# Kernel tuning notes

Measured on AMD Instinct MI355X. Metric: run time of the kernel, lower is better.

## Reference

```python
import jax, jax.numpy as jnp
import numpy as np

H = 4      # attention heads in HGTConv
DH = 32    # head dim
D = 128    # hidden size (rnn.hidden_size == hidden_size)
PAD = 0    # pad_idx


def setup_inputs() -> dict:
    key = jax.random.key(0)
    ks = jax.random.split(key, 16)
    Na = Np = 50000
    E = 800000
    V = 10000
    L = 8
    s = 0.05  # init scale keeps attention logits stable
    return {
        "tok_author": jax.random.randint(ks[0], (Na, L), 0, V),
        "tok_paper": jax.random.randint(ks[1], (Np, L), 0, V),
        "edge_ap": jax.random.randint(ks[2], (2, E), 0, Np),  # author -> paper
        "edge_pa": jax.random.randint(ks[3], (2, E), 0, Na),  # paper -> author
        "emb": jax.random.normal(ks[4], (V, D)) * s,
        "Wk": jax.random.normal(ks[5], (2, D, D)) * s,
        "Wq": jax.random.normal(ks[6], (2, D, D)) * s,
        "Wv": jax.random.normal(ks[7], (2, D, D)) * s,
        "Watt": jax.random.normal(ks[8], (2, H, DH, DH)) * s,
        "Wmsg": jax.random.normal(ks[9], (2, H, DH, DH)) * s,
        "mu": jnp.ones((2, H), jnp.float32),
        "Wout": jax.random.normal(ks[10], (2, D, D)) * s,
        "lin_w": jax.random.normal(ks[11], (D, D)) * s,
        "lin_b": jnp.zeros((D,), jnp.float32),
    }


def _st_encode(tok, emb):
    # STEncoder stand-in: embedding lookup, pad-masked mean pool, then relu_()
    e = emb[tok]                                   # [N, L, D]
    mask = (tok != PAD).astype(e.dtype)[..., None]  # [N, L, 1]
    pooled = (e * mask).sum(1) / jnp.maximum(mask.sum(1), 1.0)
    return jax.nn.relu(pooled)                     # [N, D]


def _segment_softmax(score, seg, n):
    m = jax.ops.segment_max(score, seg, num_segments=n)
    e = jnp.exp(score - m[seg])
    d = jax.ops.segment_sum(e, seg, num_segments=n)
    return e / (d[seg] + 1e-9)


def _proj(x, W):
    return (x @ W).reshape(x.shape[0], H, DH)


def _rel(k_src, v_src, q_dst, edges, Wa, Wm, mu_r, n_dst):
    # One HGT relation: per-edge key/message transform, segment-softmax attention,
    # scatter-add aggregation into destination nodes.
    src, dst = edges[0], edges[1]
    ke = jnp.einsum('ehd,hdf->ehf', k_src[src], Wa)           # [E, H, DH]
    score = (ke * q_dst[dst]).sum(-1) * mu_r / jnp.sqrt(jnp.float32(DH))  # [E, H]
    alpha = _segment_softmax(score, dst, n_dst)
    me = jnp.einsum('ehd,hdf->ehf', v_src[src], Wm)           # [E, H, DH]
    agg = jax.ops.segment_sum(alpha[..., None] * me, dst, num_segments=n_dst)
    return agg.reshape(n_dst, H * DH)


def reference(tok_author, tok_paper, edge_ap, edge_pa, emb, Wk, Wq, Wv,
              Watt, Wmsg, mu, Wout, lin_w, lin_b):
    # embed + relu per node type
    xa = _st_encode(tok_author, emb)   # [Na, D]
    xp = _st_encode(tok_paper, emb)    # [Np, D]
    Na = xa.shape[0]

    # per-node-type K/Q/V projections (type 0 = author, 1 = paper)
    ka, qa, va = _proj(xa, Wk[0]), _proj(xa, Wq[0]), _proj(xa, Wv[0])
    kp, qp, vp = _proj(xp, Wk[1]), _proj(xp, Wq[1]), _proj(xp, Wv[1])

    # only the 'author' node type feeds the output head, so we only need the
    # paper->author relation's aggregation (rel index 1)
    agg_a = _rel(kp, vp, qa, edge_pa, Watt[1], Wmsg[1], mu[1], Na)
    out_a = jax.nn.gelu(agg_a) @ Wout[0] + xa   # target-type linear + skip

    return out_a @ lin_w + lin_b
```

## Files before the change

kernel.cpp:

```cpp
#include <hip/hip_runtime.h>
#include <math.h>

#define L 8
#define FP8_SCALE 512.0f
#define FP8_INV   0.001953125f

typedef unsigned int  u32;
typedef unsigned short u16;
typedef __attribute__((ext_vector_type(8))) short bf16x8;
typedef __attribute__((ext_vector_type(4))) float f32x4;
typedef __attribute__((ext_vector_type(2))) float f32x2;

__device__ inline u16 f2bf(float x) {
    u32 u = __float_as_uint(x);
    return (u16)((u + 0x7fffu + ((u >> 16) & 1u)) >> 16);
}
__device__ inline float2 bf2f2(u32 v) {
    float2 r;
    r.x = __uint_as_float(v << 16);
    r.y = __uint_as_float(v & 0xffff0000u);
    return r;
}
__device__ inline float gelu_t(float x) {
    return 0.5f * x * (1.0f + tanhf(0.7978845608028654f *
           (x + 0.044715f * x * x * x)));
}

__device__ inline void conv_emb_body(int bid, int tid,
    const float* __restrict__ emb, u32* __restrict__ emb_bf, int n2)
{
    int i = bid * 256 + tid;
    if (i >= n2) return;
    float2 e = *(const float2*)(emb + (size_t)i * 2);
    emb_bf[i] = ((u32)f2bf(e.y) << 16) | (u32)f2bf(e.x);
}

__device__ inline void hist_body4(int bid, int tid,
    const int* __restrict__ dstI, int* __restrict__ deg, int E, int stride)
{
    int e = bid * 256 + tid;
    int e1 = e + stride, e2 = e + 2 * stride, e3 = e + 3 * stride;
    int d0 = (e  < E) ? dstI[e]  : -1;
    int d1 = (e1 < E) ? dstI[e1] : -1;
    int d2 = (e2 < E) ? dstI[e2] : -1;
    int d3 = (e3 < E) ? dstI[e3] : -1;
    if (d0 >= 0) atomicAdd(&deg[d0], 1);
    if (d1 >= 0) atomicAdd(&deg[d1], 1);
    if (d2 >= 0) atomicAdd(&deg[d2], 1);
    if (d3 >= 0) atomicAdd(&deg[d3], 1);
}

__device__ inline void fold_body(int bid, int tid,
    const float* __restrict__ Wk1, const float* __restrict__ Wq0,
    const float* __restrict__ Wv1, const float* __restrict__ Watt1,
    const float* __restrict__ Wmsg1, const float* __restrict__ Wout0,
    const float* __restrict__ lin_w,
    u16* __restrict__ wkaT, u16* __restrict__ wvmT,
    u16* __restrict__ wqT, u16* __restrict__ w1T, u16* __restrict__ lwT)
{
    int id = bid * 256 + tid;
    int which = id >> 14;
    int idx = id & 16383;
    int col = idx & 127;
    int k = idx >> 7;
    if (which == 0) {
        int h = col >> 5, f = col & 31;
        float s = 0.f;
        for (int d = 0; d < 32; ++d)
            s += Wk1[k * 128 + h * 32 + d] * Watt1[h * 1024 + d * 32 + f];
        wkaT[col * 128 + k] = f2bf(s);
    } else if (which == 1) {
        int h = col >> 5, f = col & 31;
        float s = 0.f;
        for (int d = 0; d < 32; ++d)
            s += Wv1[k * 128 + h * 32 + d] * Wmsg1[h * 1024 + d * 32 + f];
        wvmT[col * 128 + k] = f2bf(s);
    } else if (which == 2) {
        wqT[col * 128 + k] = f2bf(Wq0[k * 128 + col]);
    } else if (which == 3) {
        float s = 0.f;
        for (int d = 0; d < 128; ++d)
            s += Wout0[k * 128 + d] * lin_w[d * 128 + col];
        w1T[col * 128 + k] = f2bf(s);
    } else {
        lwT[col * 128 + k] = f2bf(lin_w[k * 128 + col]);
    }
}

__device__ inline void scan_local_body(int bid, int tid,
    const int* __restrict__ deg, int* __restrict__ locpref,
    int* __restrict__ blocksum, int Na)
{
    __shared__ int lds[256];
    int base = bid * 1024 + tid * 4;
    int4 v = {0, 0, 0, 0};
    if (base + 3 < Na) {
        v = *(const int4*)(deg + base);
    } else {
        if (base + 0 < Na) v.x = deg[base + 0];
        if (base + 1 < Na) v.y = deg[base + 1];
        if (base + 2 < Na) v.z = deg[base + 2];
        if (base + 3 < Na) v.w = deg[base + 3];
    }
    int tot = v.x + v.y + v.z + v.w;
    lds[tid] = tot;
    __syncthreads();
    for (int off = 1; off < 256; off <<= 1) {
        int u = (tid >= off) ? lds[tid - off] : 0;
        __syncthreads();
        lds[tid] += u;
        __syncthreads();
    }
    int excl = lds[tid] - tot;
    if (base < Na) {
        int4 o;
        o.x = excl;
        o.y = excl + v.x;
        o.z = o.y + v.y;
        o.w = o.z + v.z;
        if (base + 3 < Na) *(int4*)(locpref + base) = o;
        else {
            locpref[base] = o.x;
            if (base + 1 < Na) locpref[base + 1] = o.y;
            if (base + 2 < Na) locpref[base + 2] = o.z;
        }
    }
    if (tid == 255) blocksum[bid] = lds[255];
}

__device__ inline void encode_body(int bid, int tid,
    const int* __restrict__ tok_a, const int* __restrict__ tok_p,
    const uint2* __restrict__ emb_bf2,
    uint2* __restrict__ xa2, uint2* __restrict__ xp2, int Na, int Ntot)
{
    int i = bid * 256 + tid;
    int n = i >> 5, q = i & 31;
    if (n >= Ntot) return;
    const int* tok = (n < Na) ? (tok_a + (size_t)n * L)
                              : (tok_p + (size_t)(n - Na) * L);
    int4 t0 = *(const int4*)tok;
    int4 t1 = *(const int4*)(tok + 4);
    int tt[8] = {t0.x, t0.y, t0.z, t0.w, t1.x, t1.y, t1.z, t1.w};
    float ax = 0.f, ay = 0.f, az = 0.f, aw = 0.f;
    int cnt = 0;
#pragma unroll
    for (int l = 0; l < L; ++l) {
        int t = tt[l];
        if (t != 0) {
            cnt++;
            uint2 e = emb_bf2[(size_t)t * 32 + q];
            float2 e0 = bf2f2(e.x), e1 = bf2f2(e.y);
            ax += e0.x; ay += e0.y; az += e1.x; aw += e1.y;
        }
    }
    float dn = 1.0f / fmaxf((float)cnt, 1.0f);
    ax = fmaxf(ax * dn, 0.f); ay = fmaxf(ay * dn, 0.f);
    az = fmaxf(az * dn, 0.f); aw = fmaxf(aw * dn, 0.f);
    uint2 o;
    o.x = ((u32)f2bf(ay) << 16) | (u32)f2bf(ax);
    o.y = ((u32)f2bf(aw) << 16) | (u32)f2bf(az);
    if (n < Na) xa2[(size_t)n * 32 + q] = o;
    else        xp2[(size_t)(n - Na) * 32 + q] = o;
}

__device__ inline void scan_final_body(int bid, int tid,
    const int* __restrict__ locpref, const int* __restrict__ blockoff,
    int* __restrict__ rowptr, int* __restrict__ cursor, int Na)
{
    int i = bid * 256 + tid;
    if (i < Na) {
        int v = locpref[i] + blockoff[i >> 10];
        rowptr[i] = v;
        cursor[i] = v;
    }
}

__device__ inline void scatter_body4(int bid, int tid,
    const int* __restrict__ srcI, const int* __restrict__ dstI,
    int* __restrict__ cursor, int* __restrict__ csrc, int E, int stride)
{
    int e = bid * 256 + tid;
    int e1 = e + stride, e2 = e + 2 * stride, e3 = e + 3 * stride;
    int d0 = (e  < E) ? dstI[e]  : -1;
    int d1 = (e1 < E) ? dstI[e1] : -1;
    int d2 = (e2 < E) ? dstI[e2] : -1;
    int d3 = (e3 < E) ? dstI[e3] : -1;
    int s0 = (e  < E) ? srcI[e]  : 0;
    int s1 = (e1 < E) ? srcI[e1] : 0;
    int s2 = (e2 < E) ? srcI[e2] : 0;
    int s3 = (e3 < E) ? srcI[e3] : 0;
    int p0 = (d0 >= 0) ? atomicAdd(&cursor[d0], 1) : 0;
    int p1 = (d1 >= 0) ? atomicAdd(&cursor[d1], 1) : 0;
    int p2 = (d2 >= 0) ? atomicAdd(&cursor[d2], 1) : 0;
    int p3 = (d3 >= 0) ? atomicAdd(&cursor[d3], 1) : 0;
    if (d0 >= 0) csrc[p0] = s0;
    if (d1 >= 0) csrc[p1] = s1;
    if (d2 >= 0) csrc[p2] = s2;
    if (d3 >= 0) csrc[p3] = s3;
}

__global__ __launch_bounds__(256) void k_prep(
    const float* emb, u32* emb_bf, int n2,
    const int* dstI, int* deg, int E, int Bhist4, int stride,
    const float* Wk1, const float* Wq0, const float* Wv1,
    const float* Watt1, const float* Wmsg1, const float* Wout0,
    const float* lin_w, u16* wkaT, u16* wvmT, u16* wqT, u16* w1T, u16* lwT,
    int Bfold)
{
    int b = blockIdx.x, t = threadIdx.x;
    if (b < Bhist4)               hist_body4(b, t, dstI, deg, E, stride);
    else if (b < Bhist4 + Bfold)  fold_body(b - Bhist4, t, Wk1, Wq0, Wv1,
                                      Watt1, Wmsg1, Wout0, lin_w,
                                      wkaT, wvmT, wqT, w1T, lwT);
    else conv_emb_body(b - Bhist4 - Bfold, t, emb, emb_bf, n2);
}

__global__ __launch_bounds__(256) void k_scan_enc(
    const int* deg, int* locpref, int* blocksum, int Na, int BscanL,
    const int* tok_a, const int* tok_p, const uint2* emb_bf2,
    uint2* xa2, uint2* xp2, int Ntot)
{
    int b = blockIdx.x, t = threadIdx.x;
    if (b < BscanL) scan_local_body(b, t, deg, locpref, blocksum, Na);
    else encode_body(b - BscanL, t, tok_a, tok_p, emb_bf2, xa2, xp2, Na, Ntot);
}

__global__ __launch_bounds__(256) void k_scanb(
    const int* __restrict__ blocksum, int* __restrict__ blockoff,
    int* __restrict__ rowptr, int nb, int Na)
{
    __shared__ int lds[256];
    int t = threadIdx.x;
    int s = (t < nb) ? blocksum[t] : 0;
    lds[t] = s;
    __syncthreads();
    for (int off = 1; off < 256; off <<= 1) {
        int u = (t >= off) ? lds[t - off] : 0;
        __syncthreads();
        lds[t] += u;
        __syncthreads();
    }
    if (t < nb) blockoff[t] = lds[t] - s;
    if (t == 255) rowptr[Na] = lds[255];
}

__global__ __launch_bounds__(256) void k_final(
    const int* locpref, const int* blockoff, int* rowptr, int* cursor, int Na)
{
    scan_final_body(blockIdx.x, threadIdx.x, locpref, blockoff, rowptr, cursor, Na);
}

__global__ __launch_bounds__(256) void k_scat_proj(
    const int* srcI, const int* dstI, int* cursor, int* csrc, int E,
    int Bscat4, int stride,
    const u16* __restrict__ xa, const u16* __restrict__ xp,
    const u16* __restrict__ wqT, const u16* __restrict__ wkaT,
    const u16* __restrict__ wvmT,
    u16* __restrict__ qa, u32* __restrict__ km8, int Na, int Np, int gba,
    int Bproj)
{
    int b = blockIdx.x, t = threadIdx.x;
    if (b % 3 == 0) {
        int sb = b / 3;
        if (sb < Bscat4) scatter_body4(sb, t, srcI, dstI, cursor, csrc, E, stride);
        return;
    }
    int pb = (b / 3) * 2 + (b % 3 - 1);
    if (pb >= Bproj) return;

    int wave = t >> 6;
    int l = t & 63;
    int x = l & 15;
    int kb = (l >> 4) * 8;

    if (pb < gba) {
        int rbase = pb * 64 + wave * 16;
        int arow = rbase + x;
        if (arow >= Na) arow = Na - 1;
        bf16x8 af[4];
#pragma unroll
        for (int ks = 0; ks < 4; ++ks)
            af[ks] = *(const bf16x8*)(xa + (size_t)arow * 128 + ks * 32 + kb);
        f32x4 acc[8];
#pragma unroll
        for (int ct = 0; ct < 8; ++ct) acc[ct] = (f32x4){0.f, 0.f, 0.f, 0.f};
#pragma unroll
        for (int ks = 0; ks < 4; ++ks)
#pragma unroll
            for (int ct = 0; ct < 8; ++ct) {
                bf16x8 bf = *(const bf16x8*)(wqT + (size_t)(ct * 16 + x) * 128 + ks * 32 + kb);
                acc[ct] = __builtin_amdgcn_mfma_f32_16x16x32_bf16(af[ks], bf, acc[ct], 0, 0, 0);
            }
        int srow = rbase + ((l >> 4) << 2);
#pragma unroll
        for (int ct = 0; ct < 8; ++ct) {
            int col = ct * 16 + x;
#pragma unroll
            for (int r = 0; r < 4; ++r)
                if (srow + r < Na)
                    qa[(size_t)(srow + r) * 128 + col] = f2bf(acc[ct][r]);
        }
    } else {
        int b2 = pb - gba;
        int rbase = b2 * 64 + wave * 16;
        int arow = rbase + x;
        if (arow >= Np) arow = Np - 1;
        bf16x8 af[4];
#pragma unroll
        for (int ks = 0; ks < 4; ++ks)
            af[ks] = *(const bf16x8*)(xp + (size_t)arow * 128 + ks * 32 + kb);
        f32x4 kacc[8], macc[8];
#pragma unroll
        for (int ct = 0; ct < 8; ++ct) {
            kacc[ct] = (f32x4){0.f, 0.f, 0.f, 0.f};
            macc[ct] = (f32x4){0.f, 0.f, 0.f, 0.f};
        }
#pragma unroll
        for (int ks = 0; ks < 4; ++ks)
#pragma unroll
            for (int ct = 0; ct < 8; ++ct) {
                bf16x8 bk = *(const bf16x8*)(wkaT + (size_t)(ct * 16 + x) * 128 + ks * 32 + kb);
                kacc[ct] = __builtin_amdgcn_mfma_f32_16x16x32_bf16(af[ks], bk, kacc[ct], 0, 0, 0);
            }
#pragma unroll
        for (int ks = 0; ks < 4; ++ks)
#pragma unroll
            for (int ct = 0; ct < 8; ++ct) {
                bf16x8 bm = *(const bf16x8*)(wvmT + (size_t)(ct * 16 + x) * 128 + ks * 32 + kb);
                macc[ct] = __builtin_amdgcn_mfma_f32_16x16x32_bf16(af[ks], bm, macc[ct], 0, 0, 0);
            }
        int srow = rbase + ((l >> 4) << 2);
#pragma unroll
        for (int ct = 0; ct < 8; ++ct) {
#pragma unroll
            for (int r = 0; r < 4; ++r) {
                float k0 = kacc[ct][r] * FP8_SCALE;
                float k1 = __shfl_xor(k0, 1);
                float m0 = macc[ct][r] * FP8_SCALE;
                float m1 = __shfl_xor(m0, 1);
                if (!(x & 1) && (srow + r) < Np) {
                    int pk = __builtin_amdgcn_cvt_pk_fp8_f32(k0, k1, 0, false);
                    pk = __builtin_amdgcn_cvt_pk_fp8_f32(m0, m1, pk, true);
                    km8[(size_t)(srow + r) * 64 + ct * 8 + (x >> 1)] = (u32)pk;
                }
            }
        }
    }
}

__device__ inline void e_acc(u32 km, float2 qf, float muh,
                             float& dsum, float& a0, float& a1)
{
    f32x2 kf = __builtin_amdgcn_cvt_pk_f32_fp8(km, false);
    f32x2 mf = __builtin_amdgcn_cvt_pk_f32_fp8(km, true);
    float p = kf.x * qf.x + kf.y * qf.y;
    p += __shfl_xor(p, 1, 16);
    p += __shfl_xor(p, 2, 16);
    p += __shfl_xor(p, 4, 16);
    p += __shfl_xor(p, 8, 16);
    float ev = __expf(p * muh);
    dsum += ev; a0 += ev * mf.x; a1 += ev * mf.y;
}

__global__ __launch_bounds__(256) void csr_agg(
    const u32* __restrict__ km8, const u32* __restrict__ qap,
    const int* __restrict__ rowptr, const int* __restrict__ csrc,
    const float* __restrict__ mu1, u32* __restrict__ gagg, int Na)
{
    int dst = blockIdx.x * 4 + (threadIdx.x >> 6);
    if (dst >= Na) return;
    int lane = threadIdx.x & 63;
    int h = lane >> 4;
    float muh = mu1[h] * 0.17677669529663689f * FP8_INV;
    float2 qf = bf2f2(qap[(size_t)dst * 64 + lane]);

    float a0 = 0.f, a1 = 0.f, dsum = 0.f;
    int beg = rowptr[dst], end = rowptr[dst + 1];

    int i = beg;
    for (; i + 4 <= end; i += 4) {
        int s0 = csrc[i], s1 = csrc[i + 1], s2 = csrc[i + 2], s3 = csrc[i + 3];
        u32 km0 = km8[(size_t)s0 * 64 + lane];
        u32 km1 = km8[(size_t)s1 * 64 + lane];
        u32 km2 = km8[(size_t)s2 * 64 + lane];
        u32 km3 = km8[(size_t)s3 * 64 + lane];
        e_acc(km0, qf, muh, dsum, a0, a1);
        e_acc(km1, qf, muh, dsum, a0, a1);
        e_acc(km2, qf, muh, dsum, a0, a1);
        e_acc(km3, qf, muh, dsum, a0, a1);
    }
    for (; i < end; ++i) {
        u32 km0 = km8[(size_t)csrc[i] * 64 + lane];
        e_acc(km0, qf, muh, dsum, a0, a1);
    }
    float dn = dsum + 1e-9f;
    a0 = gelu_t(a0 / dn * FP8_INV);
    a1 = gelu_t(a1 / dn * FP8_INV);
    gagg[(size_t)dst * 64 + lane] = ((u32)f2bf(a1) << 16) | (u32)f2bf(a0);
}

__global__ __launch_bounds__(256) void mfma_out(
    const u16* __restrict__ A0, const u16* __restrict__ WT0,
    const u16* __restrict__ A1, const u16* __restrict__ WT1,
    const float* __restrict__ bias, float* __restrict__ Y, int N)
{
    int wave = threadIdx.x >> 6;
    int l = threadIdx.x & 63;
    int rbase = blockIdx.x * 64 + wave * 16;
    int arow = rbase + (l & 15);
    if (arow >= N) arow = N - 1;
    int kb = (l >> 4) * 8;

    f32x4 acc[8];
#pragma unroll
    for (int ct = 0; ct < 8; ++ct) acc[ct] = (f32x4){0.f, 0.f, 0.f, 0.f};

    for (int w = 0; w < 2; ++w) {
        const u16* A  = w ? A1 : A0;
        const u16* WT = w ? WT1 : WT0;
        bf16x8 af[4];
#pragma unroll
        for (int ks = 0; ks < 4; ++ks)
            af[ks] = *(const bf16x8*)(A + (size_t)arow * 128 + ks * 32 + kb);
#pragma unroll
        for (int ks = 0; ks < 4; ++ks) {
#pragma unroll
            for (int ct = 0; ct < 8; ++ct) {
                bf16x8 bf = *(const bf16x8*)(WT + (size_t)(ct * 16 + (l & 15)) * 128 + ks * 32 + kb);
                acc[ct] = __builtin_amdgcn_mfma_f32_16x16x32_bf16(af[ks], bf, acc[ct], 0, 0, 0);
            }
        }
    }
    int srow = rbase + ((l >> 4) << 2);
#pragma unroll
    for (int ct = 0; ct < 8; ++ct) {
        int col = ct * 16 + (l & 15);
        float b = bias[col];
#pragma unroll
        for (int r = 0; r < 4; ++r) {
            if (srow + r < N)
                Y[(size_t)(srow + r) * 128 + col] = acc[ct][r] + b;
        }
    }
}

extern "C" void kernel_launch(void* const* d_in, const int* in_sizes, int n_in,
                              void* d_out, int out_size, void* d_ws, size_t ws_size,
                              hipStream_t stream)
{
    const int*   tok_a   = (const int*)d_in[0];
    const int*   tok_p   = (const int*)d_in[1];
    const int*   edge_pa = (const int*)d_in[3];
    const float* emb     = (const float*)d_in[4];
    const float* Wk      = (const float*)d_in[5];
    const float* Wq      = (const float*)d_in[6];
    const float* Wv      = (const float*)d_in[7];
    const float* Watt    = (const float*)d_in[8];
    const float* Wmsg    = (const float*)d_in[9];
    const float* mu      = (const float*)d_in[10];
    const float* Wout    = (const float*)d_in[11];
    const float* lin_w   = (const float*)d_in[12];
    const float* lin_b   = (const float*)d_in[13];

    int Na = in_sizes[0] / L;
    int Np = in_sizes[1] / L;
    int E  = in_sizes[3] / 2;
    int V  = in_sizes[4] / 128;
    float* out = (float*)d_out;

    u16* xa      = (u16*)d_ws;
    u16* qa      = xa + (size_t)Na * 128;
    u16* xp      = qa + (size_t)Na * 128;
    u16* gagg    = xp + (size_t)Np * 128;
    u16* emb_bf  = gagg + (size_t)Na * 128;
    u32* km8     = (u32*)(emb_bf + (size_t)V * 128);
    int* deg     = (int*)(km8 + (size_t)Np * 64);
    int* locpref = deg + Na;
    int* rowptr  = locpref + Na;
    int* cursor  = rowptr + Na + 2;
    int* csrc    = cursor + Na;
    int* blocksum= csrc + E;
    int* blockoff= blocksum + 256;
    u16* wkaT    = (u16*)(blockoff + 256);
    u16* wvmT    = wkaT + 16384;
    u16* wqT     = wvmT + 16384;
    u16* w1T     = wqT + 16384;
    u16* lwT     = w1T + 16384;

    const int* e_src = edge_pa;
    const int* e_dst = edge_pa + E;

    int n2emb  = V * 64;
    int Bconv  = (n2emb + 255) / 256;
    int Bfold  = (5 * 16384) / 256;
    int Bhist4 = (E + 1023) / 1024;
    int stride = Bhist4 * 256;
    int nb     = (Na + 1023) / 1024;
    int Ntot   = Na + Np;
    int Benc   = ((size_t)Ntot * 32 + 255) / 256;
    int BscanF = (Na + 255) / 256;
    int gba    = (Na + 63) / 64;
    int gbp    = (Np + 63) / 64;
    int Bproj  = gba + gbp;

    (void)hipMemsetAsync(deg, 0, (size_t)Na * sizeof(int), stream);

    k_prep<<<Bhist4 + Bfold + Bconv, 256, 0, stream>>>(
        emb, (u32*)emb_bf, n2emb,
        e_dst, deg, E, Bhist4, stride,
        Wk + 16384, Wq, Wv + 16384, Watt + 4096, Wmsg + 4096, Wout, lin_w,
        wkaT, wvmT, wqT, w1T, lwT, Bfold);

    k_scan_enc<<<nb + Benc, 256, 0, stream>>>(
        deg, locpref, blocksum, Na, nb,
        tok_a, tok_p, (const uint2*)emb_bf, (uint2*)xa, (uint2*)xp, Ntot);

    k_scanb<<<1, 256, 0, stream>>>(blocksum, blockoff, rowptr, nb, Na);

    k_final<<<BscanF, 256, 0, stream>>>(locpref, blockoff, rowptr, cursor, Na);

    int Gunit = (Bhist4 > (Bproj + 1) / 2) ? Bhist4 : (Bproj + 1) / 2;
    k_scat_proj<<<3 * Gunit, 256, 0, stream>>>(
        e_src, e_dst, cursor, csrc, E, Bhist4, stride,
        xa, xp, wqT, wkaT, wvmT, qa, km8, Na, Np, gba, Bproj);

    csr_agg<<<(Na + 3) / 4, 256, 0, stream>>>(
        km8, (const u32*)qa, rowptr, csrc, mu + 4, (u32*)gagg, Na);

    mfma_out<<<gba, 256, 0, stream>>>(gagg, w1T, xa, lwT, lin_b, out, Na);
}
```

Measured before the change: 233.4 us.

## Record per-edge rank in histogram pass to make CSR scatter atomic-free

The degree histogram now stores the value returned by each atomicAdd as a per-edge rank in a scratch buffer that aliases gagg. The scatter pass then computes each slot as rowptr[dst]+rank without a second round of atomics, so the cursor array goes away. Histogram and scatter each handle 8 edges per thread instead of 4, and csr_agg gets an 8-wide unrolled gather loop. In exchange the scatter reads an extra E-sized rank array, and correctness depends on gagg not being written before csr_agg runs.

```diff
diff --git a/kernel.cpp b/kernel.cpp
--- a/kernel.cpp
+++ b/kernel.cpp
@@ -35,19 +35,25 @@
     emb_bf[i] = ((u32)f2bf(e.y) << 16) | (u32)f2bf(e.x);
 }
 
-__device__ inline void hist_body4(int bid, int tid,
-    const int* __restrict__ dstI, int* __restrict__ deg, int E, int stride)
-{
-    int e = bid * 256 + tid;
-    int e1 = e + stride, e2 = e + 2 * stride, e3 = e + 3 * stride;
-    int d0 = (e  < E) ? dstI[e]  : -1;
-    int d1 = (e1 < E) ? dstI[e1] : -1;
-    int d2 = (e2 < E) ? dstI[e2] : -1;
-    int d3 = (e3 < E) ? dstI[e3] : -1;
-    if (d0 >= 0) atomicAdd(&deg[d0], 1);
-    if (d1 >= 0) atomicAdd(&deg[d1], 1);
-    if (d2 >= 0) atomicAdd(&deg[d2], 1);
-    if (d3 >= 0) atomicAdd(&deg[d3], 1);
+__device__ inline void hist_body8(int bid, int tid,
+    const int* __restrict__ dstI, int* __restrict__ deg,
+    int* __restrict__ rank, int E, int stride)
+{
+    int e0 = bid * 256 + tid;
+    int d[8], r[8];
+#pragma unroll
+    for (int j = 0; j < 8; ++j) {
+        int e = e0 + j * stride;
+        d[j] = (e < E) ? dstI[e] : -1;
+    }
+#pragma unroll
+    for (int j = 0; j < 8; ++j)
+        r[j] = (d[j] >= 0) ? atomicAdd(&deg[d[j]], 1) : 0;
+#pragma unroll
+    for (int j = 0; j < 8; ++j) {
+        int e = e0 + j * stride;
+        if (d[j] >= 0) rank[e] = r[j];
+    }
 }
 
 __device__ inline void fold_body(int bid, int tid,
@@ -165,54 +171,50 @@
 
 __device__ inline void scan_final_body(int bid, int tid,
     const int* __restrict__ locpref, const int* __restrict__ blockoff,
-    int* __restrict__ rowptr, int* __restrict__ cursor, int Na)
+    int* __restrict__ rowptr, int Na)
 {
     int i = bid * 256 + tid;
-    if (i < Na) {
-        int v = locpref[i] + blockoff[i >> 10];
-        rowptr[i] = v;
-        cursor[i] = v;
-    }
-}
-
-__device__ inline void scatter_body4(int bid, int tid,
+    if (i < Na)
+        rowptr[i] = locpref[i] + blockoff[i >> 10];
+}
+
+__device__ inline void scatter_body8(int bid, int tid,
     const int* __restrict__ srcI, const int* __restrict__ dstI,
-    int* __restrict__ cursor, int* __restrict__ csrc, int E, int stride)
-{
-    int e = bid * 256 + tid;
-    int e1 = e + stride, e2 = e + 2 * stride, e3 = e + 3 * stride;
-    int d0 = (e  < E) ? dstI[e]  : -1;
-    int d1 = (e1 < E) ? dstI[e1] : -1;
-    int d2 = (e2 < E) ? dstI[e2] : -1;
-    int d3 = (e3 < E) ? dstI[e3] : -1;
-    int s0 = (e  < E) ? srcI[e]  : 0;
-    int s1 = (e1 < E) ? srcI[e1] : 0;
-    int s2 = (e2 < E) ? srcI[e2] : 0;
-    int s3 = (e3 < E) ? srcI[e3] : 0;
-    int p0 = (d0 >= 0) ? atomicAdd(&cursor[d0], 1) : 0;
-    int p1 = (d1 >= 0) ? atomicAdd(&cursor[d1], 1) : 0;
-    int p2 = (d2 >= 0) ? atomicAdd(&cursor[d2], 1) : 0;
-    int p3 = (d3 >= 0) ? atomicAdd(&cursor[d3], 1) : 0;
-    if (d0 >= 0) csrc[p0] = s0;
-    if (d1 >= 0) csrc[p1] = s1;
-    if (d2 >= 0) csrc[p2] = s2;
-    if (d3 >= 0) csrc[p3] = s3;
+    const int* __restrict__ rank, const int* __restrict__ rowptr,
+    int* __restrict__ csrc, int E, int stride)
+{
+    int e0 = bid * 256 + tid;
+    int d[8], s[8], r[8];
+#pragma unroll
+    for (int j = 0; j < 8; ++j) {
+        int e = e0 + j * stride;
+        d[j] = (e < E) ? dstI[e] : -1;
+        s[j] = (e < E) ? srcI[e] : 0;
+        r[j] = (e < E) ? rank[e] : 0;
+    }
+    int base[8];
+#pragma unroll
+    for (int j = 0; j < 8; ++j)
+        base[j] = (d[j] >= 0) ? rowptr[d[j]] : 0;
+#pragma unroll
+    for (int j = 0; j < 8; ++j)
+        if (d[j] >= 0) csrc[base[j] + r[j]] = s[j];
 }
 
 __global__ __launch_bounds__(256) void k_prep(
     const float* emb, u32* emb_bf, int n2,
-    const int* dstI, int* deg, int E, int Bhist4, int stride,
+    const int* dstI, int* deg, int* rank, int E, int Bhist8, int stride,
     const float* Wk1, const float* Wq0, const float* Wv1,
     const float* Watt1, const float* Wmsg1, const float* Wout0,
     const float* lin_w, u16* wkaT, u16* wvmT, u16* wqT, u16* w1T, u16* lwT,
     int Bfold)
 {
     int b = blockIdx.x, t = threadIdx.x;
-    if (b < Bhist4)               hist_body4(b, t, dstI, deg, E, stride);
-    else if (b < Bhist4 + Bfold)  fold_body(b - Bhist4, t, Wk1, Wq0, Wv1,
+    if (b < Bhist8)               hist_body8(b, t, dstI, deg, rank, E, stride);
+    else if (b < Bhist8 + Bfold)  fold_body(b - Bhist8, t, Wk1, Wq0, Wv1,
                                       Watt1, Wmsg1, Wout0, lin_w,
                                       wkaT, wvmT, wqT, w1T, lwT);
-    else conv_emb_body(b - Bhist4 - Bfold, t, emb, emb_bf, n2);
+    else conv_emb_body(b - Bhist8 - Bfold, t, emb, emb_bf, n2);
 }
 
 __global__ __launch_bounds__(256) void k_scan_enc(
@@ -245,14 +247,14 @@
 }
 
 __global__ __launch_bounds__(256) void k_final(
-    const int* locpref, const int* blockoff, int* rowptr, int* cursor, int Na)
-{
-    scan_final_body(blockIdx.x, threadIdx.x, locpref, blockoff, rowptr, cursor, Na);
+    const int* locpref, const int* blockoff, int* rowptr, int Na)
+{
+    scan_final_body(blockIdx.x, threadIdx.x, locpref, blockoff, rowptr, Na);
 }
 
 __global__ __launch_bounds__(256) void k_scat_proj(
-    const int* srcI, const int* dstI, int* cursor, int* csrc, int E,
-    int Bscat4, int stride,
+    const int* srcI, const int* dstI, const int* rank, const int* rowptr,
+    int* csrc, int E, int Bscat8, int stride,
     const u16* __restrict__ xa, const u16* __restrict__ xp,
     const u16* __restrict__ wqT, const u16* __restrict__ wkaT,
     const u16* __restrict__ wvmT,
@@ -262,7 +264,8 @@
     int b = blockIdx.x, t = threadIdx.x;
     if (b % 3 == 0) {
         int sb = b / 3;
-        if (sb < Bscat4) scatter_body4(sb, t, srcI, dstI, cursor, csrc, E, stride);
+        if (sb < Bscat8)
+            scatter_body8(sb, t, srcI, dstI, rank, rowptr, csrc, E, stride);
         return;
     }
     int pb = (b / 3) * 2 + (b % 3 - 1);
@@ -378,6 +381,16 @@
     int beg = rowptr[dst], end = rowptr[dst + 1];
 
     int i = beg;
+    for (; i + 8 <= end; i += 8) {
+        int s[8];
+        u32 km[8];
+#pragma unroll
+        for (int j = 0; j < 8; ++j) s[j] = csrc[i + j];
+#pragma unroll
+        for (int j = 0; j < 8; ++j) km[j] = km8[(size_t)s[j] * 64 + lane];
+#pragma unroll
+        for (int j = 0; j < 8; ++j) e_acc(km[j], qf, muh, dsum, a0, a1);
+    }
     for (; i + 4 <= end; i += 4) {
         int s0 = csrc[i], s1 = csrc[i + 1], s2 = csrc[i + 2], s3 = csrc[i + 3];
         u32 km0 = km8[(size_t)s0 * 64 + lane];
@@ -477,8 +490,7 @@
     int* deg     = (int*)(km8 + (size_t)Np * 64);
     int* locpref = deg + Na;
     int* rowptr  = locpref + Na;
-    int* cursor  = rowptr + Na + 2;
-    int* csrc    = cursor + Na;
+    int* csrc    = rowptr + Na + 2;
     int* blocksum= csrc + E;
     int* blockoff= blocksum + 256;
     u16* wkaT    = (u16*)(blockoff + 256);
@@ -486,6 +498,7 @@
     u16* wqT     = wvmT + 16384;
     u16* w1T     = wqT + 16384;
     u16* lwT     = w1T + 16384;
+    int* rank    = (int*)gagg;
 
     const int* e_src = edge_pa;
     const int* e_dst = edge_pa + E;
@@ -493,8 +506,8 @@
     int n2emb  = V * 64;
     int Bconv  = (n2emb + 255) / 256;
     int Bfold  = (5 * 16384) / 256;
-    int Bhist4 = (E + 1023) / 1024;
-    int stride = Bhist4 * 256;
+    int Bhist8 = (E + 2047) / 2048;
+    int hstride = Bhist8 * 256;
     int nb     = (Na + 1023) / 1024;
     int Ntot   = Na + Np;
     int Benc   = ((size_t)Ntot * 32 + 255) / 256;
@@ -502,12 +515,14 @@
     int gba    = (Na + 63) / 64;
     int gbp    = (Np + 63) / 64;
     int Bproj  = gba + gbp;
+    int Bscat8 = (E + 2047) / 2048;
+    int sstride = Bscat8 * 256;
 
     (void)hipMemsetAsync(deg, 0, (size_t)Na * sizeof(int), stream);
 
-    k_prep<<<Bhist4 + Bfold + Bconv, 256, 0, stream>>>(
+    k_prep<<<Bhist8 + Bfold + Bconv, 256, 0, stream>>>(
         emb, (u32*)emb_bf, n2emb,
-        e_dst, deg, E, Bhist4, stride,
+        e_dst, deg, rank, E, Bhist8, hstride,
         Wk + 16384, Wq, Wv + 16384, Watt + 4096, Wmsg + 4096, Wout, lin_w,
         wkaT, wvmT, wqT, w1T, lwT, Bfold);
 
@@ -517,11 +532,11 @@
 
     k_scanb<<<1, 256, 0, stream>>>(blocksum, blockoff, rowptr, nb, Na);
 
-    k_final<<<BscanF, 256, 0, stream>>>(locpref, blockoff, rowptr, cursor, Na);
-
-    int Gunit = (Bhist4 > (Bproj + 1) / 2) ? Bhist4 : (Bproj + 1) / 2;
+    k_final<<<BscanF, 256, 0, stream>>>(locpref, blockoff, rowptr, Na);
+
+    int Gunit = (Bscat8 > (Bproj + 1) / 2) ? Bscat8 : (Bproj + 1) / 2;
     k_scat_proj<<<3 * Gunit, 256, 0, stream>>>(
-        e_src, e_dst, cursor, csrc, E, Bhist4, stride,
+        e_src, e_dst, rank, rowptr, csrc, E, Bscat8, sstride,
         xa, xp, wqT, wkaT, wvmT, qa, km8, Na, Np, gba, Bproj);
 
     csr_agg<<<(Na + 3) / 4, 256, 0, stream>>>(
```

After: 213.1 us. -8.7%, faster.
